# Optimization experiments

Hardware: AMD Instinct MI355X
Metric: run time of the kernel (lower is better)

## Reference

```python
import jax, jax.numpy as jnp
import numpy as np

B, L, C, H, W, R = 1, 8, 16, 240, 480, 8
MID = C // 2          # HamiltonianGenerator mid channels
SE_MID = max(C // 16, 4)

SOBEL_X = jnp.array([[-1., 0., 1.], [-2., 0., 2.], [-1., 0., 1.]], jnp.float32).reshape(1, 1, 3, 3)
SOBEL_Y = jnp.array([[-1., -2., -1.], [0., 0., 0.], [1., 2., 1.]], jnp.float32).reshape(1, 1, 3, 3)


def _conv2d(x, w, b=None, padding='SAME'):
    y = jax.lax.conv_general_dilated(x, w, (1, 1), padding,
                                     dimension_numbers=('NCHW', 'OIHW', 'NCHW'))
    return y if b is None else y + b[None, :, None, None]


def _flow_field(x, w1, b1, w2, b2):
    # x: [B,L,C,H,W] -> flow [B,L,2,H,W] (HamiltonianGenerator)
    b_, l_, c_, h_, w_ = x.shape
    xf = x.reshape(b_ * l_, c_, h_, w_)
    f = jax.nn.silu(_conv2d(xf, w1, b1))
    f = _conv2d(f, w2, b2)                      # [N,2,H,W]
    phi, psi = f[:, :1], f[:, 1:]

    def grads(p):
        p = jnp.pad(p, ((0, 0), (0, 0), (0, 0), (1, 1)), mode='wrap')   # circular in W
        p = jnp.pad(p, ((0, 0), (0, 0), (1, 1), (0, 0)), mode='edge')   # replicate in H
        return (_conv2d(p, SOBEL_X, padding='VALID'),
                _conv2d(p, SOBEL_Y, padding='VALID'))

    gx_phi, gy_phi = grads(phi)
    gx_psi, gy_psi = grads(psi)
    lat = jnp.linspace(-np.pi / 2, np.pi / 2, h_).reshape(1, 1, h_, 1)
    metric = 1.0 / (jnp.cos(lat) + 1e-6)
    u = gx_phi * metric - gy_psi
    v = gy_phi + gx_psi * metric
    return jnp.tanh(jnp.concatenate([u, v], axis=1)).reshape(b_, l_, 2, h_, w_)


def _grid_sample_border(im, grid):
    # im: [C,H,W,R], grid: [H,W,2] in [-1,1]; bilinear, border pad, align_corners=False
    c_, h_, w_, r_ = im.shape
    xp = (grid[..., 0] + 1.0) * (w_ * 0.5) - 0.5
    yp = (grid[..., 1] + 1.0) * (h_ * 0.5) - 0.5
    xp = jnp.clip(xp, 0.0, w_ - 1.0)
    yp = jnp.clip(yp, 0.0, h_ - 1.0)
    x0f = jnp.floor(xp); y0f = jnp.floor(yp)
    wx = (xp - x0f)[None, :, :, None]
    wy = (yp - y0f)[None, :, :, None]
    x0 = x0f.astype(jnp.int32); y0 = y0f.astype(jnp.int32)
    x1 = jnp.minimum(x0 + 1, w_ - 1); y1 = jnp.minimum(y0 + 1, h_ - 1)
    v00 = im[:, y0, x0, :]; v01 = im[:, y0, x1, :]
    v10 = im[:, y1, x0, :]; v11 = im[:, y1, x1, :]
    top = v00 * (1 - wx) + v01 * wx
    bot = v10 * (1 - wx) + v11 * wx
    return top * (1 - wy) + bot * wy


def _forward(x, h0, listT, hw1, hb1, hw2, hb2, sw1, sb1, sw2, sb2):
    b_, l_, c_, h_, w_ = x.shape
    flow = _flow_field(x, hw1, hb1, hw2, hb2)           # [B,L,2,H,W]
    gy, gx = jnp.meshgrid(jnp.linspace(-1.0, 1.0, h_),
                          jnp.linspace(-1.0, 1.0, w_), indexing='ij')
    base_grid = jnp.stack([gx, gy], axis=-1)            # [H,W,2]
    sample = jax.vmap(_grid_sample_border, in_axes=(0, 0))

    def se_gate(xf):
        # LatitudeAwareSE on [B,C,H,W]: pool over W, MLP over C per latitude
        y = xf.mean(axis=-1)                                              # [B,C,H]
        y = jax.nn.silu(jnp.einsum('bch,mc->bmh', y, sw1) + sb1[None, :, None])
        y = jax.nn.sigmoid(jnp.einsum('bmh,cm->bch', y, sw2) + sb2[None, :, None])
        return xf * y[..., None]

    def step(h, inp):
        flow_t, dt_t, x_t = inp                          # [B,2,H,W], [B], [B,C,H,W]
        disp = flow_t * dt_t[:, None, None, None]
        grid = base_grid[None] - jnp.moveaxis(disp, 1, -1)   # [B,H,W,2]
        h = sample(h, grid)                              # LieTransport advection
        h = h + x_t[..., None]                           # inject current frame
        y = se_gate(h.mean(axis=-1))                     # readout over rank + SE gate
        return h, y

    xs = (jnp.moveaxis(flow, 1, 0), listT.T, jnp.moveaxis(x, 1, 0))
    _, ys = jax.lax.scan(step, h0, xs)                   # ys: [L,B,C,H,W]
    return jnp.moveaxis(ys, 0, 1)                        # [B,L,C,H,W]


def setup_inputs() -> dict:
    key = jax.random.key(0)
    ks = jax.random.split(key, 8)
    return {
        'x': jax.random.normal(ks[0], (B, L, C, H, W), jnp.float32),
        'h0': jax.random.normal(ks[1], (B, C, H, W, R), jnp.float32),
        'listT': jax.random.uniform(ks[2], (B, L), jnp.float32, 0.1, 1.0),
        'ham_w1': jax.random.normal(ks[3], (MID, C, 3, 3), jnp.float32) * 0.08,
        'ham_b1': jnp.zeros((MID,), jnp.float32),
        'ham_w2': jax.random.normal(ks[4], (2, MID, 3, 3), jnp.float32) * 0.08,
        'ham_b2': jnp.zeros((2,), jnp.float32),
        'se_w1': jax.random.normal(ks[5], (SE_MID, C), jnp.float32) * 0.25,
        'se_b1': jnp.zeros((SE_MID,), jnp.float32),
        'se_w2': jax.random.normal(ks[6], (C, SE_MID), jnp.float32) * 0.25,
        'se_b2': jnp.zeros((C,), jnp.float32),
    }


def reference(x, h0, listT, ham_w1, ham_b1, ham_w2, ham_b2, se_w1, se_b1, se_w2, se_b2):
    return _forward(x, h0, listT, ham_w1, ham_b1, ham_w2, ham_b2, se_w1, se_b1, se_w2, se_b2)
```

## Files before the change

kernel.cpp:

```cpp
#include <hip/hip_runtime.h>
#include <math.h>

constexpr int Lq = 8, Cq = 16, Hq = 240, Wq = 480, MIDq = 8, SEM = 4;
constexpr int HWq = Hq * Wq;

__device__ __forceinline__ float sigmoidf_(float v) { return 1.0f / (1.0f + expf(-v)); }

__global__ void k_conv1(const float* __restrict__ x, const float* __restrict__ w1,
                        const float* __restrict__ b1, float* __restrict__ f1) {
    int b = blockIdx.x;
    int l = b & 7, y = b >> 3;
    int t = threadIdx.x;
    if (t >= Wq / 4) return;
    int xi = t * 4;
    float acc[MIDq][4];
#pragma unroll
    for (int m = 0; m < MIDq; m++) {
        float bv = b1[m];
#pragma unroll
        for (int o = 0; o < 4; o++) acc[m][o] = bv;
    }
#pragma unroll 2
    for (int ic = 0; ic < Cq; ic++) {
        const float* xin = x + (size_t)(l * Cq + ic) * HWq;
        const float* wrow = w1 + ic * 9;
#pragma unroll
        for (int r = 0; r < 3; r++) {
            int yy = y + r - 1;
            if (yy < 0 || yy >= Hq) continue;
            const float* rp = xin + yy * Wq;
            float4 mid = *(const float4*)(rp + xi);
            float lft = (xi > 0) ? rp[xi - 1] : 0.f;
            float rgt = (xi + 4 < Wq) ? rp[xi + 4] : 0.f;
            float in6[6] = {lft, mid.x, mid.y, mid.z, mid.w, rgt};
#pragma unroll
            for (int m = 0; m < MIDq; m++) {
                const float* wp = wrow + m * (Cq * 9) + r * 3;
                float w0 = wp[0], w1v = wp[1], w2 = wp[2];
#pragma unroll
                for (int o = 0; o < 4; o++)
                    acc[m][o] = fmaf(w0, in6[o],
                                fmaf(w1v, in6[o + 1],
                                fmaf(w2, in6[o + 2], acc[m][o])));
            }
        }
    }
    size_t rowoff = (size_t)y * Wq + xi;
#pragma unroll
    for (int m = 0; m < MIDq; m++) {
        float4 v;
        float a0 = acc[m][0], a1 = acc[m][1], a2 = acc[m][2], a3 = acc[m][3];
        v.x = a0 * sigmoidf_(a0);
        v.y = a1 * sigmoidf_(a1);
        v.z = a2 * sigmoidf_(a2);
        v.w = a3 * sigmoidf_(a3);
        *(float4*)(f1 + (size_t)(l * MIDq + m) * HWq + rowoff) = v;
    }
}

__global__ void k_conv2(const float* __restrict__ f1, const float* __restrict__ w2,
                        const float* __restrict__ b2, float* __restrict__ f) {
    int b = blockIdx.x;
    int l = b & 7, y = b >> 3;
    int t = threadIdx.x;
    if (t >= Wq / 4) return;
    int xi = t * 4;
    float acc[2][4];
#pragma unroll
    for (int m = 0; m < 2; m++) {
        float bv = b2[m];
#pragma unroll
        for (int o = 0; o < 4; o++) acc[m][o] = bv;
    }
#pragma unroll 2
    for (int ic = 0; ic < MIDq; ic++) {
        const float* fin = f1 + (size_t)(l * MIDq + ic) * HWq;
        const float* wrow = w2 + ic * 9;
#pragma unroll
        for (int r = 0; r < 3; r++) {
            int yy = y + r - 1;
            if (yy < 0 || yy >= Hq) continue;
            const float* rp = fin + yy * Wq;
            float4 mid = *(const float4*)(rp + xi);
            float lft = (xi > 0) ? rp[xi - 1] : 0.f;
            float rgt = (xi + 4 < Wq) ? rp[xi + 4] : 0.f;
            float in6[6] = {lft, mid.x, mid.y, mid.z, mid.w, rgt};
#pragma unroll
            for (int m = 0; m < 2; m++) {
                const float* wp = wrow + m * (MIDq * 9) + r * 3;
                float w0 = wp[0], w1v = wp[1], w2v = wp[2];
#pragma unroll
                for (int o = 0; o < 4; o++)
                    acc[m][o] = fmaf(w0, in6[o],
                                fmaf(w1v, in6[o + 1],
                                fmaf(w2v, in6[o + 2], acc[m][o])));
            }
        }
    }
    size_t rowoff = (size_t)y * Wq + xi;
#pragma unroll
    for (int m = 0; m < 2; m++) {
        float4 v = {acc[m][0], acc[m][1], acc[m][2], acc[m][3]};
        *(float4*)(f + (size_t)(l * 2 + m) * HWq + rowoff) = v;
    }
}

__global__ void k_flow(const float* __restrict__ f, float* __restrict__ flow) {
    int idx = blockIdx.x * blockDim.x + threadIdx.x;
    if (idx >= Lq * HWq) return;
    int l = idx / HWq, rem = idx % HWq, y = rem / Wq, x = rem % Wq;
    const float* phi = f + (size_t)(l * 2 + 0) * HWq;
    const float* psi = f + (size_t)(l * 2 + 1) * HWq;
    float ph[3][3], ps[3][3];
#pragma unroll
    for (int i = 0; i < 3; i++) {
        int yy = y + i - 1;
        yy = yy < 0 ? 0 : (yy >= Hq ? Hq - 1 : yy);
#pragma unroll
        for (int j = 0; j < 3; j++) {
            int xx = x + j - 1;
            xx = (xx + Wq) % Wq;
            ph[i][j] = phi[yy * Wq + xx];
            ps[i][j] = psi[yy * Wq + xx];
        }
    }
    float gxp = (ph[0][2] - ph[0][0]) + 2.f * (ph[1][2] - ph[1][0]) + (ph[2][2] - ph[2][0]);
    float gyp = (ph[2][0] + 2.f * ph[2][1] + ph[2][2]) - (ph[0][0] + 2.f * ph[0][1] + ph[0][2]);
    float gxs = (ps[0][2] - ps[0][0]) + 2.f * (ps[1][2] - ps[1][0]) + (ps[2][2] - ps[2][0]);
    float gys = (ps[2][0] + 2.f * ps[2][1] + ps[2][2]) - (ps[0][0] + 2.f * ps[0][1] + ps[0][2]);
    float latf = (float)(-M_PI * 0.5 + (double)y * (M_PI / (double)(Hq - 1)));
    float metric = (float)(1.0 / (cos((double)latf) + 1e-6));
    float u = gxp * metric - gys;
    float v = gyp + gxs * metric;
    flow[(size_t)(l * 2 + 0) * HWq + rem] = tanhf(u);
    flow[(size_t)(l * 2 + 1) * HWq + rem] = tanhf(v);
}

__global__ void k_m0(const float* __restrict__ h0, float* __restrict__ m0) {
    int px = blockIdx.x * 256 + threadIdx.x;
    const float4* h4 = (const float4*)h0;
    float4* mp = (float4*)(m0 + (size_t)px * Cq);
#pragma unroll
    for (int cq = 0; cq < 4; cq++) {
        float vals[4];
#pragma unroll
        for (int cc = 0; cc < 4; cc++) {
            int c = cq * 4 + cc;
            float4 a = h4[(size_t)(c * HWq + px) * 2];
            float4 b = h4[(size_t)(c * HWq + px) * 2 + 1];
            vals[cc] = (a.x + a.y + a.z + a.w + b.x + b.y + b.z + b.w) * 0.125f;
        }
        float4 o = {vals[0], vals[1], vals[2], vals[3]};
        mp[cq] = o;
    }
}

__global__ __launch_bounds__(1024) void k_step(const float* __restrict__ min_,
                       float* __restrict__ mout, const float* __restrict__ flow_l,
                       const float* __restrict__ xl, const float* __restrict__ listT,
                       int l,
                       const float* __restrict__ sw1, const float* __restrict__ sb1,
                       const float* __restrict__ sw2, const float* __restrict__ sb2,
                       float* __restrict__ out_l) {
    constexpr int STR = 17;
    __shared__ float sm[Wq * STR];
    __shared__ float csum[Cq];
    __shared__ float zl[SEM];
    __shared__ float gl[Cq];

    int y = blockIdx.x;
    int t = threadIdx.x;
    int wave = t >> 6, lane = t & 63;
    bool act = t < 2 * Wq;
    int px = act ? (t >> 1) : (Wq - 1);
    int half = t & 1;
    int c0 = half * 8;

    float dt = listT[l];
    float mn[8];
    {
        float u = flow_l[y * Wq + px];
        float v = flow_l[HWq + y * Wq + px];
        float gx = (px * (2.0f / (Wq - 1)) - 1.0f) - u * dt;
        float gy = (y * (2.0f / (Hq - 1)) - 1.0f) - v * dt;
        float xp = fminf(fmaxf((gx + 1.0f) * (Wq * 0.5f) - 0.5f, 0.0f), (float)(Wq - 1));
        float yp = fminf(fmaxf((gy + 1.0f) * (Hq * 0.5f) - 0.5f, 0.0f), (float)(Hq - 1));
        float x0f = floorf(xp), y0f = floorf(yp);
        float wx = xp - x0f, wy = yp - y0f;
        int x0 = (int)x0f, y0 = (int)y0f;
        int x1 = min(x0 + 1, Wq - 1), y1 = min(y0 + 1, Hq - 1);
        const float4* m4 = (const float4*)min_;
        size_t b00 = (size_t)(y0 * Wq + x0) * 4 + (half * 2);
        size_t b01 = (size_t)(y0 * Wq + x1) * 4 + (half * 2);
        size_t b10 = (size_t)(y1 * Wq + x0) * 4 + (half * 2);
        size_t b11 = (size_t)(y1 * Wq + x1) * 4 + (half * 2);
        float4 A0 = m4[b00], A1 = m4[b00 + 1];
        float4 B0 = m4[b01], B1 = m4[b01 + 1];
        float4 C0 = m4[b10], C1 = m4[b10 + 1];
        float4 D0 = m4[b11], D1 = m4[b11 + 1];
        float w00 = (1.f - wx) * (1.f - wy), w01 = wx * (1.f - wy);
        float w10 = (1.f - wx) * wy, w11 = wx * wy;
        const float* xb = xl + y * Wq + px;
        float xv[8];
#pragma unroll
        for (int j = 0; j < 8; j++) xv[j] = xb[(size_t)(c0 + j) * HWq];
        mn[0] = w00 * A0.x + w01 * B0.x + w10 * C0.x + w11 * D0.x + xv[0];
        mn[1] = w00 * A0.y + w01 * B0.y + w10 * C0.y + w11 * D0.y + xv[1];
        mn[2] = w00 * A0.z + w01 * B0.z + w10 * C0.z + w11 * D0.z + xv[2];
        mn[3] = w00 * A0.w + w01 * B0.w + w10 * C0.w + w11 * D0.w + xv[3];
        mn[4] = w00 * A1.x + w01 * B1.x + w10 * C1.x + w11 * D1.x + xv[4];
        mn[5] = w00 * A1.y + w01 * B1.y + w10 * C1.y + w11 * D1.y + xv[5];
        mn[6] = w00 * A1.z + w01 * B1.z + w10 * C1.z + w11 * D1.z + xv[6];
        mn[7] = w00 * A1.w + w01 * B1.w + w10 * C1.w + w11 * D1.w + xv[7];
    }
    if (act) {
        float4* mo = (float4*)(mout + (size_t)(y * Wq + px) * Cq + c0);
        float4 o0 = {mn[0], mn[1], mn[2], mn[3]};
        float4 o1 = {mn[4], mn[5], mn[6], mn[7]};
        mo[0] = o0;
        mo[1] = o1;
#pragma unroll
        for (int j = 0; j < 8; j++) sm[px * STR + c0 + j] = mn[j];
    }
    __syncthreads();
    {
        float s = 0.f;
#pragma unroll
        for (int k = 0; k < 8; k++) {
            int p = k * 64 + lane;
            if (p < Wq) s += sm[p * STR + wave];
        }
#pragma unroll
        for (int off = 32; off > 0; off >>= 1) s += __shfl_down(s, off, 64);
        if (lane == 0) csum[wave] = s;
    }
    __syncthreads();
    if (t < SEM) {
        float a = sb1[t];
#pragma unroll
        for (int i = 0; i < Cq; i++) a = fmaf(sw1[t * Cq + i], csum[i] * (1.0f / Wq), a);
        zl[t] = a * sigmoidf_(a);
    }
    __syncthreads();
    if (t < Cq) {
        float a = sb2[t];
#pragma unroll
        for (int m = 0; m < SEM; m++) a = fmaf(sw2[t * SEM + m], zl[m], a);
        gl[t] = sigmoidf_(a);
    }
    __syncthreads();
    if (act) {
        float* ob = out_l + y * Wq + px;
#pragma unroll
        for (int j = 0; j < 8; j++)
            ob[(size_t)(c0 + j) * HWq] = mn[j] * gl[c0 + j];
    }
}

extern "C" void kernel_launch(void* const* d_in, const int* in_sizes, int n_in,
                              void* d_out, int out_size, void* d_ws, size_t ws_size,
                              hipStream_t stream) {
    const float* x = (const float*)d_in[0];
    const float* h0 = (const float*)d_in[1];
    const float* listT = (const float*)d_in[2];
    const float* hw1 = (const float*)d_in[3];
    const float* hb1 = (const float*)d_in[4];
    const float* hw2 = (const float*)d_in[5];
    const float* hb2 = (const float*)d_in[6];
    const float* sw1 = (const float*)d_in[7];
    const float* sb1 = (const float*)d_in[8];
    const float* sw2 = (const float*)d_in[9];
    const float* sb2 = (const float*)d_in[10];
    float* out = (float*)d_out;
    char* ws = (char*)d_ws;

    size_t off = 0;
    float* flow = (float*)(ws + off); off += sizeof(float) * (size_t)Lq * 2 * HWq;
    float* f    = (float*)(ws + off); off += sizeof(float) * (size_t)Lq * 2 * HWq;
    float* f1   = (float*)(ws + off); off += sizeof(float) * (size_t)Lq * MIDq * HWq;
    float* mA   = (float*)(ws + off); off += sizeof(float) * (size_t)HWq * Cq;
    float* mB   = (float*)(ws + off); off += sizeof(float) * (size_t)HWq * Cq;

    k_conv1<<<Lq * Hq, 128, 0, stream>>>(x, hw1, hb1, f1);
    k_conv2<<<Lq * Hq, 128, 0, stream>>>(f1, hw2, hb2, f);
    k_flow<<<(Lq * HWq + 255) / 256, 256, 0, stream>>>(f, flow);
    k_m0<<<HWq / 256, 256, 0, stream>>>(h0, mA);

    float* bufs[2] = {mA, mB};
    for (int l = 0; l < Lq; l++) {
        float* min_ = bufs[l & 1];
        float* mout = bufs[(l + 1) & 1];
        k_step<<<Hq, 1024, 0, stream>>>(min_, mout, flow + (size_t)l * 2 * HWq,
                                        x + (size_t)l * Cq * HWq, listT, l,
                                        sw1, sb1, sw2, sb2,
                                        out + (size_t)l * Cq * HWq);
    }
}
```

Before: 164.7 us.

## Share conv halo via wave shuffles, batch channel loads, compute SE gate per thread

New measurement: 219.1 us. 1.33x slower.

```diff
diff --git a/kernel.cpp b/kernel.cpp
--- a/kernel.cpp
+++ b/kernel.cpp
@@ -11,8 +11,9 @@
     int b = blockIdx.x;
     int l = b & 7, y = b >> 3;
     int t = threadIdx.x;
-    if (t >= Wq / 4) return;
-    int xi = t * 4;
+    int lane = t & 63;
+    int tc = t < 120 ? t : 119;
+    int xi = tc * 4;
     float acc[MIDq][4];
 #pragma unroll
     for (int m = 0; m < MIDq; m++) {
@@ -20,41 +21,48 @@
 #pragma unroll
         for (int o = 0; o < 4; o++) acc[m][o] = bv;
     }
-#pragma unroll 2
-    for (int ic = 0; ic < Cq; ic++) {
-        const float* xin = x + (size_t)(l * Cq + ic) * HWq;
-        const float* wrow = w1 + ic * 9;
-#pragma unroll
-        for (int r = 0; r < 3; r++) {
-            int yy = y + r - 1;
-            if (yy < 0 || yy >= Hq) continue;
-            const float* rp = xin + yy * Wq;
-            float4 mid = *(const float4*)(rp + xi);
-            float lft = (xi > 0) ? rp[xi - 1] : 0.f;
-            float rgt = (xi + 4 < Wq) ? rp[xi + 4] : 0.f;
-            float in6[6] = {lft, mid.x, mid.y, mid.z, mid.w, rgt};
+    const float* xbase = x + (size_t)l * Cq * HWq;
+#pragma unroll
+    for (int r = 0; r < 3; r++) {
+        int yy = y + r - 1;
+        if (yy < 0 || yy >= Hq) continue;
+        const float* rowp = xbase + (size_t)yy * Wq;
+        float4 mid[Cq];
+#pragma unroll
+        for (int ic = 0; ic < Cq; ic++)
+            mid[ic] = *(const float4*)(rowp + (size_t)ic * HWq + xi);
+#pragma unroll
+        for (int ic = 0; ic < Cq; ic++) {
+            float lft = __shfl_up(mid[ic].w, 1, 64);
+            if (lane == 0) lft = (xi == 0) ? 0.f : rowp[(size_t)ic * HWq + xi - 1];
+            float rgt = __shfl_down(mid[ic].x, 1, 64);
+            if (lane == 63) rgt = (xi + 4 < Wq) ? rowp[(size_t)ic * HWq + xi + 4] : 0.f;
+            if (xi + 4 >= Wq) rgt = 0.f;
+            float in6[6] = {lft, mid[ic].x, mid[ic].y, mid[ic].z, mid[ic].w, rgt};
 #pragma unroll
             for (int m = 0; m < MIDq; m++) {
-                const float* wp = wrow + m * (Cq * 9) + r * 3;
-                float w0 = wp[0], w1v = wp[1], w2 = wp[2];
+                const float* wp = w1 + ((size_t)m * Cq + ic) * 9 + r * 3;
+                float w0 = wp[0], w1v = wp[1], w2v = wp[2];
 #pragma unroll
                 for (int o = 0; o < 4; o++)
                     acc[m][o] = fmaf(w0, in6[o],
                                 fmaf(w1v, in6[o + 1],
-                                fmaf(w2, in6[o + 2], acc[m][o])));
+                                fmaf(w2v, in6[o + 2], acc[m][o])));
             }
         }
     }
-    size_t rowoff = (size_t)y * Wq + xi;
-#pragma unroll
-    for (int m = 0; m < MIDq; m++) {
-        float4 v;
-        float a0 = acc[m][0], a1 = acc[m][1], a2 = acc[m][2], a3 = acc[m][3];
-        v.x = a0 * sigmoidf_(a0);
-        v.y = a1 * sigmoidf_(a1);
-        v.z = a2 * sigmoidf_(a2);
-        v.w = a3 * sigmoidf_(a3);
-        *(float4*)(f1 + (size_t)(l * MIDq + m) * HWq + rowoff) = v;
+    if (t < 120) {
+        size_t rowoff = (size_t)y * Wq + xi;
+#pragma unroll
+        for (int m = 0; m < MIDq; m++) {
+            float4 v;
+            float a0 = acc[m][0], a1 = acc[m][1], a2 = acc[m][2], a3 = acc[m][3];
+            v.x = a0 * sigmoidf_(a0);
+            v.y = a1 * sigmoidf_(a1);
+            v.z = a2 * sigmoidf_(a2);
+            v.w = a3 * sigmoidf_(a3);
+            *(float4*)(f1 + (size_t)(l * MIDq + m) * HWq + rowoff) = v;
+        }
     }
 }
 
@@ -63,8 +71,9 @@
     int b = blockIdx.x;
     int l = b & 7, y = b >> 3;
     int t = threadIdx.x;
-    if (t >= Wq / 4) return;
-    int xi = t * 4;
+    int lane = t & 63;
+    int tc = t < 120 ? t : 119;
+    int xi = tc * 4;
     float acc[2][4];
 #pragma unroll
     for (int m = 0; m < 2; m++) {
@@ -72,22 +81,27 @@
 #pragma unroll
         for (int o = 0; o < 4; o++) acc[m][o] = bv;
     }
-#pragma unroll 2
-    for (int ic = 0; ic < MIDq; ic++) {
-        const float* fin = f1 + (size_t)(l * MIDq + ic) * HWq;
-        const float* wrow = w2 + ic * 9;
-#pragma unroll
-        for (int r = 0; r < 3; r++) {
-            int yy = y + r - 1;
-            if (yy < 0 || yy >= Hq) continue;
-            const float* rp = fin + yy * Wq;
-            float4 mid = *(const float4*)(rp + xi);
-            float lft = (xi > 0) ? rp[xi - 1] : 0.f;
-            float rgt = (xi + 4 < Wq) ? rp[xi + 4] : 0.f;
-            float in6[6] = {lft, mid.x, mid.y, mid.z, mid.w, rgt};
+    const float* fbase = f1 + (size_t)l * MIDq * HWq;
+#pragma unroll
+    for (int r = 0; r < 3; r++) {
+        int yy = y + r - 1;
+        if (yy < 0 || yy >= Hq) continue;
+        const float* rowp = fbase + (size_t)yy * Wq;
+        float4 mid[MIDq];
+#pragma unroll
+        for (int ic = 0; ic < MIDq; ic++)
+            mid[ic] = *(const float4*)(rowp + (size_t)ic * HWq + xi);
+#pragma unroll
+        for (int ic = 0; ic < MIDq; ic++) {
+            float lft = __shfl_up(mid[ic].w, 1, 64);
+            if (lane == 0) lft = (xi == 0) ? 0.f : rowp[(size_t)ic * HWq + xi - 1];
+            float rgt = __shfl_down(mid[ic].x, 1, 64);
+            if (lane == 63) rgt = (xi + 4 < Wq) ? rowp[(size_t)ic * HWq + xi + 4] : 0.f;
+            if (xi + 4 >= Wq) rgt = 0.f;
+            float in6[6] = {lft, mid[ic].x, mid[ic].y, mid[ic].z, mid[ic].w, rgt};
 #pragma unroll
             for (int m = 0; m < 2; m++) {
-                const float* wp = wrow + m * (MIDq * 9) + r * 3;
+                const float* wp = w2 + ((size_t)m * MIDq + ic) * 9 + r * 3;
                 float w0 = wp[0], w1v = wp[1], w2v = wp[2];
 #pragma unroll
                 for (int o = 0; o < 4; o++)
@@ -97,11 +111,13 @@
             }
         }
     }
-    size_t rowoff = (size_t)y * Wq + xi;
-#pragma unroll
-    for (int m = 0; m < 2; m++) {
-        float4 v = {acc[m][0], acc[m][1], acc[m][2], acc[m][3]};
-        *(float4*)(f + (size_t)(l * 2 + m) * HWq + rowoff) = v;
+    if (t < 120) {
+        size_t rowoff = (size_t)y * Wq + xi;
+#pragma unroll
+        for (int m = 0; m < 2; m++) {
+            float4 v = {acc[m][0], acc[m][1], acc[m][2], acc[m][3]};
+            *(float4*)(f + (size_t)(l * 2 + m) * HWq + rowoff) = v;
+        }
     }
 }
 
@@ -165,8 +181,6 @@
     constexpr int STR = 17;
     __shared__ float sm[Wq * STR];
     __shared__ float csum[Cq];
-    __shared__ float zl[SEM];
-    __shared__ float gl[Cq];
 
     int y = blockIdx.x;
     int t = threadIdx.x;
@@ -235,25 +249,26 @@
         if (lane == 0) csum[wave] = s;
     }
     __syncthreads();
-    if (t < SEM) {
-        float a = sb1[t];
-#pragma unroll
-        for (int i = 0; i < Cq; i++) a = fmaf(sw1[t * Cq + i], csum[i] * (1.0f / Wq), a);
-        zl[t] = a * sigmoidf_(a);
-    }
-    __syncthreads();
-    if (t < Cq) {
-        float a = sb2[t];
-#pragma unroll
-        for (int m = 0; m < SEM; m++) a = fmaf(sw2[t * SEM + m], zl[m], a);
-        gl[t] = sigmoidf_(a);
-    }
-    __syncthreads();
     if (act) {
+        float ym[Cq];
+#pragma unroll
+        for (int i = 0; i < Cq; i++) ym[i] = csum[i] * (1.0f / Wq);
+        float z[SEM];
+#pragma unroll
+        for (int mm = 0; mm < SEM; mm++) {
+            float a = sb1[mm];
+#pragma unroll
+            for (int i = 0; i < Cq; i++) a = fmaf(sw1[mm * Cq + i], ym[i], a);
+            z[mm] = a * sigmoidf_(a);
+        }
         float* ob = out_l + y * Wq + px;
 #pragma unroll
-        for (int j = 0; j < 8; j++)
-            ob[(size_t)(c0 + j) * HWq] = mn[j] * gl[c0 + j];
+        for (int j = 0; j < 8; j++) {
+            float a = sb2[c0 + j];
+#pragma unroll
+            for (int mm = 0; mm < SEM; mm++) a = fmaf(sw2[(c0 + j) * SEM + mm], z[mm], a);
+            ob[(size_t)(c0 + j) * HWq] = mn[j] * sigmoidf_(a);
+        }
     }
 }
 
```
